# Kernel optimization log

Measured on AMD Instinct MI355X. Metric: run time of the kernel, lower is better.

Reference implementation:

```python
import jax, jax.numpy as jnp
import numpy as np

LN_EPS = 1e-5

def layer_norm(x, w, b):
    mu = jnp.mean(x, axis=-1, keepdims=True)
    var = jnp.mean(jnp.square(x - mu), axis=-1, keepdims=True)
    return (x - mu) * jax.lax.rsqrt(var + LN_EPS) * w + b

def adaptive_mask_np(aa, bb, ada_para=0.2):
    # True = disallowed (matches torch ~bool mask). Static shapes -> numpy.
    adaptive_num = int(bb * ada_para)
    cc = bb // aa
    i = np.arange(aa)
    start = i * cc
    end = start + cc + adaptive_num
    over = end > bb - 1
    start = np.where(over, np.maximum(start - (end - (bb - 1)), 0), start)
    end = np.where(over, bb, end)
    cols = np.arange(bb)
    allowed = (cols[None, :] >= start[:, None]) & (cols[None, :] < end[:, None])
    return jnp.asarray(~allowed)  # [aa, bb] bool

def setup_inputs() -> dict:
    key = jax.random.key(0)
    ks = jax.random.split(key, 20)
    Lq, Lk, B, d, dff = 512, 4096, 4, 512, 2048
    s = lambda k, shape: jax.random.normal(k, shape, dtype=jnp.float32) * 0.02
    inp = {
        'tgt': jax.random.normal(ks[0], (Lq, B, d), dtype=jnp.float32),
        'memory': jax.random.normal(ks[1], (Lk, B, d), dtype=jnp.float32),
        'Wq': s(ks[2], (d, d)), 'bq': jnp.zeros((d,), jnp.float32),
        'Wk': s(ks[3], (d, d)), 'bk': jnp.zeros((d,), jnp.float32),
        'Wv': s(ks[4], (d, d)), 'bv': jnp.zeros((d,), jnp.float32),
        'Wo': s(ks[5], (d, d)), 'bo': jnp.zeros((d,), jnp.float32),
        'W1': s(ks[6], (dff, d)), 'b1': jnp.zeros((dff,), jnp.float32),
        'W2': s(ks[7], (d, dff)), 'b2': jnp.zeros((d,), jnp.float32),
        'ln1_w': jnp.ones((d,), jnp.float32), 'ln1_b': jnp.zeros((d,), jnp.float32),
        'ln2_w': jnp.ones((d,), jnp.float32), 'ln2_b': jnp.zeros((d,), jnp.float32),
        'ln3_w': jnp.ones((d,), jnp.float32), 'ln3_b': jnp.zeros((d,), jnp.float32),
        'ln4_w': jnp.ones((d,), jnp.float32), 'ln4_b': jnp.zeros((d,), jnp.float32),
    }
    return inp

def reference(tgt, memory, Wq, bq, Wk, bk, Wv, bv, Wo, bo, W1, b1, W2, b2,
              ln1_w, ln1_b, ln2_w, ln2_b, ln3_w, ln3_b, ln4_w, ln4_b):
    Lq, B, d = tgt.shape
    Lk = memory.shape[0]
    H = 8
    hd = d // H
    scale = 1.0 / jnp.sqrt(jnp.asarray(hd, tgt.dtype))

    t = layer_norm(tgt, ln1_w, ln1_b)      # [Lq,B,d]
    m = layer_norm(memory, ln2_w, ln2_b)   # [Lk,B,d]

    mask = adaptive_mask_np(Lq, Lk, 0.2)   # [Lq,Lk] bool, True=masked

    q = (t @ Wq.T + bq).reshape(Lq, B, H, hd)
    k = (m @ Wk.T + bk).reshape(Lk, B, H, hd)
    v = (m @ Wv.T + bv).reshape(Lk, B, H, hd)

    scores = jnp.einsum('qbhd,kbhd->bhqk', q * scale, k)
    scores = jnp.where(mask[None, None], -jnp.inf, scores)
    p = jax.nn.softmax(scores, axis=-1)                   # [B,H,Lq,Lk]
    attn_weights = jnp.mean(p, axis=1)                    # [B,Lq,Lk] (avg over heads)

    ctx = jnp.einsum('bhqk,kbhd->qbhd', p, v).reshape(Lq, B, d)
    tgt2 = ctx @ Wo.T + bo

    x = t + tgt2                       # dropout1 = identity (eval)
    x = layer_norm(x, ln3_w, ln3_b)
    ff = jax.nn.relu(x @ W1.T + b1) @ W2.T + b2
    x = x + ff                         # dropout2 = identity (eval)
    x = layer_norm(x, ln4_w, ln4_b)
    return (x, attn_weights)
```

## Files before the change

### kernel.cpp

```cpp
#include <hip/hip_runtime.h>
#include <hip/hip_bf16.h>

typedef __hip_bfloat16 bf16_t;
typedef __bf16 bf16x8 __attribute__((ext_vector_type(8)));
typedef float f32x4 __attribute__((ext_vector_type(4)));

#define LQ 512
#define LK 4096
#define BATCH 4
#define DMODEL 512
#define NHEAD 8
#define HEADDIM 64
#define DFF 2048
#define LN_EPS 1e-5f

__device__ inline float tofl(float x) { return x; }
__device__ inline float tofl(bf16_t x) { return __bfloat162float(x); }
__device__ inline void stfl(float* p, float v) { *p = v; }
__device__ inline void stfl(bf16_t* p, float v) { *p = __float2bfloat16(v); }

__device__ __forceinline__ void gld_lds16(const bf16_t* g, void* lds_base) {
    __builtin_amdgcn_global_load_lds(
        (const __attribute__((address_space(1))) uint32_t*)g,
        (__attribute__((address_space(3))) uint32_t*)lds_base, 16, 0, 0);
}

__global__ void prep_kernel(const float* __restrict__ s0, const float* __restrict__ s1,
                            const float* __restrict__ s2, const float* __restrict__ s3,
                            const float* __restrict__ s4, const float* __restrict__ s5,
                            bf16_t* __restrict__ wqkvo, bf16_t* __restrict__ w1bf,
                            bf16_t* __restrict__ w2bf, float* __restrict__ zbuf) {
    int bid = blockIdx.x;
    int tid = threadIdx.x;
    if (bid < 3072) {
        int t = bid * 256 + tid;
        int which = t >> 16;
        int idx = (t & 65535) * 4;
        const float* s; bf16_t* d;
        if (which < 4) {
            s = (which == 0 ? s0 : which == 1 ? s1 : which == 2 ? s2 : s3) ;
            d = wqkvo + (size_t)which * 262144;
        } else if (which < 8) {
            s = s4 + (size_t)(which - 4) * 262144;
            d = w1bf + (size_t)(which - 4) * 262144;
        } else {
            s = s5 + (size_t)(which - 8) * 262144;
            d = w2bf + (size_t)(which - 8) * 262144;
        }
        float4 v = *(const float4*)(s + idx);
        d[idx + 0] = __float2bfloat16(v.x);
        d[idx + 1] = __float2bfloat16(v.y);
        d[idx + 2] = __float2bfloat16(v.z);
        d[idx + 3] = __float2bfloat16(v.w);
    } else {
        size_t i = ((size_t)(bid - 3072) * 256 + tid) * 4;
        float4 z = {0.f, 0.f, 0.f, 0.f};
        *(float4*)(zbuf + i) = z;
    }
}

template <typename TOUT, bool DUAL>
__global__ void ln_kernel(const float* __restrict__ in, const float* __restrict__ w,
                          const float* __restrict__ b, TOUT* __restrict__ out1,
                          float* __restrict__ out2) {
    __shared__ float red[256];
    const int row = blockIdx.x;
    const int tid = threadIdx.x;
    const float* x = in + (size_t)row * DMODEL;
    float v0 = x[tid];
    float v1 = x[tid + 256];

    red[tid] = v0 + v1;
    __syncthreads();
    for (int s = 128; s > 0; s >>= 1) { if (tid < s) red[tid] += red[tid + s]; __syncthreads(); }
    float mu = red[0] * (1.0f / DMODEL);
    __syncthreads();

    float d0 = v0 - mu, d1 = v1 - mu;
    red[tid] = d0 * d0 + d1 * d1;
    __syncthreads();
    for (int s = 128; s > 0; s >>= 1) { if (tid < s) red[tid] += red[tid + s]; __syncthreads(); }
    float inv = rsqrtf(red[0] * (1.0f / DMODEL) + LN_EPS);

    float r0 = d0 * inv * w[tid] + b[tid];
    float r1 = d1 * inv * w[tid + 256] + b[tid + 256];
    TOUT* o = out1 + (size_t)row * DMODEL;
    stfl(&o[tid], r0);
    stfl(&o[tid + 256], r1);
    if (DUAL) {
        float* o2 = out2 + (size_t)row * DMODEL;
        o2[tid] = r0;
        o2[tid + 256] = r1;
    }
}

__global__ void ln12_kernel(const float* __restrict__ tgt, const float* __restrict__ memory,
                            const float* __restrict__ w1, const float* __restrict__ b1,
                            const float* __restrict__ w2, const float* __restrict__ b2,
                            bf16_t* __restrict__ t_bf, float* __restrict__ t_f32,
                            bf16_t* __restrict__ m_buf) {
    __shared__ float red[256];
    const int row = blockIdx.x;
    const int tid = threadIdx.x;
    const float* in; const float* w; const float* b;
    bf16_t* o1; float* o2; bool dual;
    if (row < 2048) {
        in = tgt + (size_t)row * DMODEL; w = w1; b = b1;
        o1 = t_bf + (size_t)row * DMODEL; o2 = t_f32 + (size_t)row * DMODEL; dual = true;
    } else {
        int r2 = row - 2048;
        in = memory + (size_t)r2 * DMODEL; w = w2; b = b2;
        o1 = m_buf + (size_t)r2 * DMODEL; o2 = nullptr; dual = false;
    }
    float v0 = in[tid];
    float v1 = in[tid + 256];
    red[tid] = v0 + v1;
    __syncthreads();
    for (int s = 128; s > 0; s >>= 1) { if (tid < s) red[tid] += red[tid + s]; __syncthreads(); }
    float mu = red[0] * (1.0f / DMODEL);
    __syncthreads();
    float d0 = v0 - mu, d1 = v1 - mu;
    red[tid] = d0 * d0 + d1 * d1;
    __syncthreads();
    for (int s = 128; s > 0; s >>= 1) { if (tid < s) red[tid] += red[tid + s]; __syncthreads(); }
    float inv = rsqrtf(red[0] * (1.0f / DMODEL) + LN_EPS);
    float r0 = d0 * inv * w[tid] + b[tid];
    float r1 = d1 * inv * w[tid + 256] + b[tid + 256];
    o1[tid] = __float2bfloat16(r0);
    o1[tid + 256] = __float2bfloat16(r1);
    if (dual) {
        o2[tid] = r0;
        o2[tid + 256] = r1;
    }
}

template <int TN, typename TC, bool RELU, bool RESID>
__global__ __launch_bounds__(256) void gemm_mfma(
        const bf16_t* __restrict__ A, const bf16_t* __restrict__ B,
        const float* __restrict__ bias, const float* __restrict__ resid,
        TC* __restrict__ C, int M, int N, int K) {
    __shared__ uint4 As4[1024];
    __shared__ uint4 Bs4[TN * 8];

    const int tid = threadIdx.x;
    const int lane = tid & 63;
    const int wave = tid >> 6;
    const int row16 = lane & 15;
    const int quad = lane >> 4;
    const int n0 = blockIdx.x * TN;
    const int m0 = blockIdx.y * 128;

    constexpr int MI = (TN == 128) ? 4 : 2;
    const int wy = (TN == 128) ? (wave >> 1) : wave;
    const int wx = (TN == 128) ? (wave & 1) : 0;
    const int m_base = wy * ((TN == 128) ? 64 : 32);
    const int n_base = wx * 64;

    const int rr = lane >> 3;
    const int kc = (lane & 7) ^ rr;
    const int kx = row16 & 7;

    const bf16_t* AsE = (const bf16_t*)As4;
    const bf16_t* BsE = (const bf16_t*)Bs4;

    f32x4 acc[MI][4] = {};

    for (int k0 = 0; k0 < K; k0 += 64) {
#pragma unroll
        for (int it = 0; it < 4; it++) {
            int issue = it * 4 + wave;
            int r = issue * 8 + rr;
            gld_lds16(A + (size_t)(m0 + r) * K + k0 + kc * 8, &As4[issue * 64]);
        }
#pragma unroll
        for (int it = 0; it < TN / 32; it++) {
            int issue = it * 4 + wave;
            int r = issue * 8 + rr;
            gld_lds16(B + (size_t)(n0 + r) * K + k0 + kc * 8, &Bs4[issue * 64]);
        }
        __syncthreads();
#pragma unroll
        for (int s = 0; s < 2; s++) {
            const int kq = s * 4 + quad;
            const int kcs = (kq ^ kx) * 8;
            bf16x8 af[MI], bfr[4];
#pragma unroll
            for (int i = 0; i < MI; i++)
                af[i] = *(const bf16x8*)&AsE[(m_base + i * 16 + row16) * 64 + kcs];
#pragma unroll
            for (int j = 0; j < 4; j++)
                bfr[j] = *(const bf16x8*)&BsE[(n_base + j * 16 + row16) * 64 + kcs];
#pragma unroll
            for (int i = 0; i < MI; i++)
#pragma unroll
                for (int j = 0; j < 4; j++)
                    acc[i][j] = __builtin_amdgcn_mfma_f32_16x16x32_bf16(af[i], bfr[j], acc[i][j], 0, 0, 0);
        }
        __syncthreads();
    }

#pragma unroll
    for (int i = 0; i < MI; i++) {
#pragma unroll
        for (int j = 0; j < 4; j++) {
            int col = n0 + n_base + j * 16 + row16;
            float bsv = bias[col];
#pragma unroll
            for (int r = 0; r < 4; r++) {
                int row = m0 + m_base + i * 16 + quad * 4 + r;
                float val = acc[i][j][r] + bsv;
                if (RESID) val += resid[(size_t)row * N + col];
                if (RELU) val = fmaxf(val, 0.0f);
                stfl(&C[(size_t)row * N + col], val);
            }
        }
    }
}

__global__ __launch_bounds__(256) void transpose_kv(const bf16_t* __restrict__ kb,
                                                    bf16_t* __restrict__ kT) {
    __shared__ bf16_t tile[64][80];
    const int kt = blockIdx.x * 64;
    const int ct = blockIdx.y * 64;
    const int b  = blockIdx.z;
    const int t = threadIdx.x;
    {
        int kl = t >> 2, cl = (t & 3) * 16;
        const bf16_t* src = kb + ((size_t)(kt + kl) * 4 + b) * 512 + ct + cl;
        *(uint4*)&tile[kl][cl]     = *(const uint4*)src;
        *(uint4*)&tile[kl][cl + 8] = *(const uint4*)(src + 8);
    }
    __syncthreads();
    {
        int cl2 = t >> 2, ks = (t & 3) * 16;
        __attribute__((aligned(16))) bf16_t vals[16];
#pragma unroll
        for (int j = 0; j < 16; j++) vals[j] = tile[ks + j][cl2];
        bf16_t* dst = kT + ((size_t)b * 512 + ct + cl2) * 4096 + kt + ks;
        *(uint4*)dst       = *(const uint4*)&vals[0];
        *(uint4*)(dst + 8) = *(const uint4*)&vals[8];
    }
}

__global__ __launch_bounds__(512, 4) void attn_mfma(
        const bf16_t* __restrict__ qb,
        const bf16_t* __restrict__ kb,
        const bf16_t* __restrict__ vT,
        bf16_t* __restrict__ ctx,
        float* __restrict__ attn_out) {
    const int d = blockIdx.x;
    const int g = d & 7;
    const int b = g >> 1;
    const int qhalf = g & 1;
    const int i_in = d >> 3;
    const int hg = i_in & 1;
    const int qt = qhalf * 32 + (i_in >> 1);
    const int q0 = qt * 8;
    const int tid = threadIdx.x;
    const int lane = tid & 63;
    const int w8 = tid >> 6;
    const int hw = w8 & 3;
    const int half = w8 >> 2;
    const int h = hg * 4 + hw;
    const int hoffg = h * HEADDIM;
    const int hl = hw * HEADDIM;
    const int row16 = lane & 15;
    const int quad = lane >> 4;

    __align__(16) __shared__ bf16_t Qs[8][264];
    __align__(16) __shared__ bf16_t Zrow[904];
    __align__(16) __shared__ bf16_t Ps[4][8][904];
    __shared__ float Ls2[2][4][8];

    int us; { int s = q0 * 8, e = s + 827; if (e > 4095) s = 3268; us = s; }
    int sq[4], eq[4];
#pragma unroll
    for (int r = 0; r < 4; r++) {
        int ql = quad * 4 + r;
        if (ql < 8) {
            int s = (q0 + ql) * 8, e = s + 827;
            if (e > 4095) { s = 3268; e = 4096; }
            sq[r] = s; eq[r] = e;
        } else { sq[r] = 0; eq[r] = 0; }
    }

    if (tid < 256) {
        int r = tid >> 5, coff = (tid & 31) * 8;
        *(uint4*)&Qs[r][coff] =
            *(const uint4*)(qb + ((size_t)(q0 + r) * 4 + b) * 512 + hg * 256 + coff);
        if (tid < 113) { uint4 z = {0, 0, 0, 0}; *(uint4*)&Zrow[tid * 8] = z; }
    }
    __syncthreads();

    const bf16_t* q0p = (row16 < 8) ? &Qs[row16][hl + quad * 8] : &Zrow[0];
    const bf16_t* q1p = (row16 < 8) ? &Qs[row16][hl + 32 + quad * 8] : &Zrow[8];
    const bf16x8 aq0 = *(const bf16x8*)q0p;
    const bf16x8 aq1 = *(const bf16x8*)q1p;

    float l[4] = {0.f, 0.f, 0.f, 0.f};
    const int it0 = half * 28;
#pragma unroll 4
    for (int it = it0; it < it0 + 28; ++it) {
        const int c = it >> 3;
        const int t8 = it & 7;
        const int cb = c * 128;
        int key = us + cb + t8 * 16 + row16;
        int key_eff = key > 4095 ? 4095 : key;
        const bf16_t* kr = kb + (size_t)key_eff * 2048 + (size_t)b * 512 + hoffg;
        bf16x8 bk0 = *(const bf16x8*)(kr + quad * 8);
        bf16x8 bk1 = *(const bf16x8*)(kr + 32 + quad * 8);
        f32x4 acc = {};
        acc = __builtin_amdgcn_mfma_f32_16x16x32_bf16(aq0, bk0, acc, 0, 0, 0);
        acc = __builtin_amdgcn_mfma_f32_16x16x32_bf16(aq1, bk1, acc, 0, 0, 0);
#pragma unroll
        for (int r = 0; r < 4; r++) {
            int ql = quad * 4 + r;
            bool valid = (key >= sq[r]) && (key < eq[r]);
            float p = valid ? __expf(0.125f * acc[r]) : 0.0f;
            l[r] += p;
            if (ql < 8) Ps[hw][ql][cb + t8 * 16 + row16] = __float2bfloat16(p);
        }
    }
#pragma unroll
    for (int off = 1; off < 16; off <<= 1) {
#pragma unroll
        for (int r = 0; r < 4; r++) l[r] += __shfl_xor(l[r], off, 64);
    }
    if (row16 == 0) {
#pragma unroll
        for (int r = 0; r < 4; r++) {
            int ql = quad * 4 + r;
            if (ql < 8) Ls2[half][hw][ql] = l[r];
        }
    }
    __syncthreads();

    float linv[4];
#pragma unroll
    for (int r = 0; r < 4; r++) {
        int ql = quad * 4 + r;
        linv[r] = (ql < 8) ? 1.0f / (Ls2[0][hw][ql] + Ls2[1][hw][ql]) : 0.0f;
    }

    {
        int qq = w8;
        float ls0 = 0.125f / (Ls2[0][0][qq] + Ls2[1][0][qq]);
        float ls1 = 0.125f / (Ls2[0][1][qq] + Ls2[1][1][qq]);
        float ls2 = 0.125f / (Ls2[0][2][qq] + Ls2[1][2][qq]);
        float ls3 = 0.125f / (Ls2[0][3][qq] + Ls2[1][3][qq]);
        float* base = attn_out + ((size_t)b * LQ + q0 + qq) * LK + us;
        const int cmax = LK - us;
        for (int col = lane; col < 896; col += 64) {
            if (col < cmax) {
                float s = ls0 * tofl(Ps[0][qq][col]) + ls1 * tofl(Ps[1][qq][col]) +
                          ls2 * tofl(Ps[2][qq][col]) + ls3 * tofl(Ps[3][qq][col]);
                atomicAdd(base + col, s);
            }
        }
    }

    f32x4 o[4] = {};
    const int pv0 = half * 14;
#pragma unroll 2
    for (int it = pv0; it < pv0 + 14; ++it) {
        const int c = it >> 2;
        const int kt2 = it & 3;
        const int cb = c * 128;
        const bf16_t* ap_src = (row16 < 8) ? &Ps[hw][row16][cb + kt2 * 32 + quad * 8]
                                           : &Zrow[0];
        bf16x8 ap = *(const bf16x8*)ap_src;
#pragma unroll
        for (int nt = 0; nt < 4; nt++) {
            const bf16_t* vr = vT + ((size_t)b * 512 + hoffg + nt * 16 + row16) * 4096
                               + us + cb + kt2 * 32 + quad * 8;
            bf16x8 bv = *(const bf16x8*)vr;
            o[nt] = __builtin_amdgcn_mfma_f32_16x16x32_bf16(ap, bv, o[nt], 0, 0, 0);
        }
    }

    __syncthreads();
    float* Osum = (float*)Ps;
    if (half == 1) {
#pragma unroll
        for (int nt = 0; nt < 4; nt++) {
#pragma unroll
            for (int r = 0; r < 4; r++) {
                int ql = quad * 4 + r;
                if (ql < 8) Osum[(hw * 8 + ql) * 65 + nt * 16 + row16] = o[nt][r];
            }
        }
    }
    __syncthreads();
    if (half == 0) {
#pragma unroll
        for (int nt = 0; nt < 4; nt++) {
#pragma unroll
            for (int r = 0; r < 4; r++) {
                int ql = quad * 4 + r;
                if (ql < 8) {
                    float tot = o[nt][r] + Osum[(hw * 8 + ql) * 65 + nt * 16 + row16];
                    ctx[((size_t)(q0 + ql) * 4 + b) * 512 + hoffg + nt * 16 + row16] =
                        __float2bfloat16(tot * linv[r]);
                }
            }
        }
    }
}

extern "C" void kernel_launch(void* const* d_in, const int* in_sizes, int n_in,
                              void* d_out, int out_size, void* d_ws, size_t ws_size,
                              hipStream_t stream) {
    const float* tgt    = (const float*)d_in[0];
    const float* memory = (const float*)d_in[1];
    const float* Wq = (const float*)d_in[2];
    const float* bq = (const float*)d_in[3];
    const float* Wk = (const float*)d_in[4];
    const float* bk = (const float*)d_in[5];
    const float* Wv = (const float*)d_in[6];
    const float* bv = (const float*)d_in[7];
    const float* Wo = (const float*)d_in[8];
    const float* bo = (const float*)d_in[9];
    const float* W1 = (const float*)d_in[10];
    const float* b1 = (const float*)d_in[11];
    const float* W2 = (const float*)d_in[12];
    const float* b2 = (const float*)d_in[13];
    const float* ln1w = (const float*)d_in[14];
    const float* ln1b = (const float*)d_in[15];
    const float* ln2w = (const float*)d_in[16];
    const float* ln2b = (const float*)d_in[17];
    const float* ln3w = (const float*)d_in[18];
    const float* ln3b = (const float*)d_in[19];
    const float* ln4w = (const float*)d_in[20];
    const float* ln4b = (const float*)d_in[21];

    const size_t M1 = (size_t)LQ * BATCH;
    const size_t M2 = (size_t)LK * BATCH;
    const size_t SZ1 = M1 * DMODEL;

    char* wsb = (char*)d_ws;
    const size_t MB = 1 << 20;
    bf16_t* m_buf   = (bf16_t*)(wsb + 0 * MB);
    bf16_t* vT_buf  = (bf16_t*)(wsb + 0 * MB);
    bf16_t* h_buf   = (bf16_t*)(wsb + 0 * MB);
    float*  xln_f   = (float*)(wsb + 8 * MB);
    float*  x2_buf  = (float*)(wsb + 12 * MB);
    bf16_t* k_buf   = (bf16_t*)(wsb + 16 * MB);
    bf16_t* v_buf   = (bf16_t*)(wsb + 32 * MB);
    float*  xres    = (float*)(wsb + 32 * MB);
    bf16_t* t_bf    = (bf16_t*)(wsb + 48 * MB);
    bf16_t* xln_bf  = (bf16_t*)(wsb + 48 * MB);
    float*  t_f32   = (float*)(wsb + 50 * MB);
    bf16_t* q_bf    = (bf16_t*)(wsb + 54 * MB);
    bf16_t* W2_bf   = (bf16_t*)(wsb + 56 * MB);
    bf16_t* ctx_buf = (bf16_t*)(wsb + 58 * MB);
    bf16_t* wqkvo   = (bf16_t*)(wsb + 60 * MB);
    bf16_t* W1_bf   = (bf16_t*)(wsb + 62 * MB);

    bf16_t* Wq_bf = wqkvo;
    bf16_t* Wk_bf = wqkvo + 262144;
    bf16_t* Wv_bf = wqkvo + 2 * 262144;
    bf16_t* Wo_bf = wqkvo + 3 * 262144;

    float* out_x    = (float*)d_out;
    float* out_attn = out_x + SZ1;

    prep_kernel<<<dim3(11264), dim3(256), 0, stream>>>(
        Wq, Wk, Wv, Wo, W1, W2, wqkvo, W1_bf, W2_bf, out_attn);

    ln12_kernel<<<dim3(M1 + M2), dim3(256), 0, stream>>>(
        tgt, memory, ln1w, ln1b, ln2w, ln2b, t_bf, t_f32, m_buf);

    gemm_mfma<64, bf16_t, false, false><<<dim3(8, 16), dim3(256), 0, stream>>>(
        t_bf, Wq_bf, bq, nullptr, q_bf, M1, DMODEL, DMODEL);
    gemm_mfma<128, bf16_t, false, false><<<dim3(4, 128), dim3(256), 0, stream>>>(
        m_buf, Wk_bf, bk, nullptr, k_buf, M2, DMODEL, DMODEL);
    gemm_mfma<128, bf16_t, false, false><<<dim3(4, 128), dim3(256), 0, stream>>>(
        m_buf, Wv_bf, bv, nullptr, v_buf, M2, DMODEL, DMODEL);

    transpose_kv<<<dim3(64, 8, 4), dim3(256), 0, stream>>>(v_buf, vT_buf);

    attn_mfma<<<dim3(512), dim3(512), 0, stream>>>(q_bf, k_buf, vT_buf, ctx_buf, out_attn);

    gemm_mfma<64, float, false, true><<<dim3(8, 16), dim3(256), 0, stream>>>(
        ctx_buf, Wo_bf, bo, t_f32, xres, M1, DMODEL, DMODEL);

    ln_kernel<bf16_t, true><<<dim3(M1), dim3(256), 0, stream>>>(xres, ln3w, ln3b, xln_bf, xln_f);

    gemm_mfma<128, bf16_t, true, false><<<dim3(16, 16), dim3(256), 0, stream>>>(
        xln_bf, W1_bf, b1, nullptr, h_buf, M1, DFF, DMODEL);

    gemm_mfma<64, float, false, true><<<dim3(8, 16), dim3(256), 0, stream>>>(
        h_buf, W2_bf, b2, xln_f, x2_buf, M1, DMODEL, DFF);

    ln_kernel<float, false><<<dim3(M1), dim3(256), 0, stream>>>(x2_buf, ln4w, ln4b, out_x, nullptr);
}
```

Measured before the change: 331.1 us.

## Prefetch K and V tiles into register ring buffers and reorder attention sync

The QK^T loop is fully unrolled and keeps an 8-deep register ring of K fragments, issuing loads for iteration j+8 while computing iteration j. The P·V loop does the same with a 4-deep ring of V fragments. The P·V pass now runs before the block-wide barrier and the head-averaged atomic write of attention weights. This removes one barrier and is meant to hide global-load latency behind MFMA work. In exchange it uses many more VGPRs (about 128 for the buffers), which may lower occupancy.

```diff
diff --git a/kernel.cpp b/kernel.cpp
--- a/kernel.cpp
+++ b/kernel.cpp
@@ -297,28 +297,40 @@
     const bf16x8 aq0 = *(const bf16x8*)q0p;
     const bf16x8 aq1 = *(const bf16x8*)q1p;
 
+    const int it0 = half * 28;
+    const bf16_t* kb_base = kb + (size_t)b * 512 + hoffg + quad * 8;
+    auto kaddr = [&](int it) -> const bf16_t* {
+        int key = us + it * 16 + row16;
+        int key_eff = key > 4095 ? 4095 : key;
+        return kb_base + (size_t)key_eff * 2048;
+    };
+    bf16x8 kbuf0[8], kbuf1[8];
+#pragma unroll
+    for (int j = 0; j < 8; ++j) {
+        const bf16_t* p = kaddr(it0 + j);
+        kbuf0[j] = *(const bf16x8*)p;
+        kbuf1[j] = *(const bf16x8*)(p + 32);
+    }
     float l[4] = {0.f, 0.f, 0.f, 0.f};
-    const int it0 = half * 28;
-#pragma unroll 4
-    for (int it = it0; it < it0 + 28; ++it) {
-        const int c = it >> 3;
-        const int t8 = it & 7;
-        const int cb = c * 128;
-        int key = us + cb + t8 * 16 + row16;
-        int key_eff = key > 4095 ? 4095 : key;
-        const bf16_t* kr = kb + (size_t)key_eff * 2048 + (size_t)b * 512 + hoffg;
-        bf16x8 bk0 = *(const bf16x8*)(kr + quad * 8);
-        bf16x8 bk1 = *(const bf16x8*)(kr + 32 + quad * 8);
+#pragma unroll
+    for (int j = 0; j < 28; ++j) {
+        const int it = it0 + j;
         f32x4 acc = {};
-        acc = __builtin_amdgcn_mfma_f32_16x16x32_bf16(aq0, bk0, acc, 0, 0, 0);
-        acc = __builtin_amdgcn_mfma_f32_16x16x32_bf16(aq1, bk1, acc, 0, 0, 0);
+        acc = __builtin_amdgcn_mfma_f32_16x16x32_bf16(aq0, kbuf0[j & 7], acc, 0, 0, 0);
+        acc = __builtin_amdgcn_mfma_f32_16x16x32_bf16(aq1, kbuf1[j & 7], acc, 0, 0, 0);
+        if (j + 8 < 28) {
+            const bf16_t* p = kaddr(it + 8);
+            kbuf0[j & 7] = *(const bf16x8*)p;
+            kbuf1[j & 7] = *(const bf16x8*)(p + 32);
+        }
+        const int key = us + it * 16 + row16;
 #pragma unroll
         for (int r = 0; r < 4; r++) {
             int ql = quad * 4 + r;
             bool valid = (key >= sq[r]) && (key < eq[r]);
             float p = valid ? __expf(0.125f * acc[r]) : 0.0f;
             l[r] += p;
-            if (ql < 8) Ps[hw][ql][cb + t8 * 16 + row16] = __float2bfloat16(p);
+            if (ql < 8) Ps[hw][ql][it * 16 + row16] = __float2bfloat16(p);
         }
     }
 #pragma unroll
@@ -333,14 +345,35 @@
             if (ql < 8) Ls2[half][hw][ql] = l[r];
         }
     }
-    __syncthreads();
-
-    float linv[4];
-#pragma unroll
-    for (int r = 0; r < 4; r++) {
-        int ql = quad * 4 + r;
-        linv[r] = (ql < 8) ? 1.0f / (Ls2[0][hw][ql] + Ls2[1][hw][ql]) : 0.0f;
-    }
+
+    const int pv0 = half * 14;
+    auto vaddr = [&](int it, int nt) -> const bf16_t* {
+        return vT + ((size_t)b * 512 + hoffg + nt * 16 + row16) * 4096
+               + us + it * 32 + quad * 8;
+    };
+    bf16x8 vbuf[4][4];
+#pragma unroll
+    for (int j = 0; j < 4; ++j)
+#pragma unroll
+        for (int nt = 0; nt < 4; ++nt) vbuf[j][nt] = *(const bf16x8*)vaddr(pv0 + j, nt);
+
+    f32x4 o[4] = {};
+#pragma unroll
+    for (int j = 0; j < 14; ++j) {
+        const int it = pv0 + j;
+        const bf16_t* ap_src = (row16 < 8) ? &Ps[hw][row16][it * 32 + quad * 8]
+                                           : &Zrow[0];
+        bf16x8 ap = *(const bf16x8*)ap_src;
+#pragma unroll
+        for (int nt = 0; nt < 4; ++nt)
+            o[nt] = __builtin_amdgcn_mfma_f32_16x16x32_bf16(ap, vbuf[j & 3][nt], o[nt], 0, 0, 0);
+        if (j + 4 < 14) {
+#pragma unroll
+            for (int nt = 0; nt < 4; ++nt) vbuf[j & 3][nt] = *(const bf16x8*)vaddr(it + 4, nt);
+        }
+    }
+
+    __syncthreads();
 
     {
         int qq = w8;
@@ -359,23 +392,11 @@
         }
     }
 
-    f32x4 o[4] = {};
-    const int pv0 = half * 14;
-#pragma unroll 2
-    for (int it = pv0; it < pv0 + 14; ++it) {
-        const int c = it >> 2;
-        const int kt2 = it & 3;
-        const int cb = c * 128;
-        const bf16_t* ap_src = (row16 < 8) ? &Ps[hw][row16][cb + kt2 * 32 + quad * 8]
-                                           : &Zrow[0];
-        bf16x8 ap = *(const bf16x8*)ap_src;
-#pragma unroll
-        for (int nt = 0; nt < 4; nt++) {
-            const bf16_t* vr = vT + ((size_t)b * 512 + hoffg + nt * 16 + row16) * 4096
-                               + us + cb + kt2 * 32 + quad * 8;
-            bf16x8 bv = *(const bf16x8*)vr;
-            o[nt] = __builtin_amdgcn_mfma_f32_16x16x32_bf16(ap, bv, o[nt], 0, 0, 0);
-        }
+    float linv[4];
+#pragma unroll
+    for (int r = 0; r < 4; r++) {
+        int ql = quad * 4 + r;
+        linv[r] = (ql < 8) ? 1.0f / (Ls2[0][hw][ql] + Ls2[1][hw][ql]) : 0.0f;
     }
 
     __syncthreads();
```

Measured after the change: 357.2 us. 1.08x slower.
